# Performance work log

Hardware: AMD Instinct MI355X
Metric: run time of the kernel (lower is better)

Reference implementation:

```python
import jax, jax.numpy as jnp
import numpy as np

N_SAMPLES = 32768


def fft_shift(a, shift):
    n = a.shape[-1]
    shift_samples = shift * (n / 3.0)  # trailing dim of shift is 1 -> broadcasts over coeffs
    pad = [(0, 0)] * (a.ndim - 1) + [(0, 2 * n)]
    spec = jnp.fft.rfft(jnp.pad(a, pad), axis=-1, norm='ortho')
    n_coeffs = spec.shape[-1]
    phase = jnp.arange(n_coeffs) * (2j * jnp.pi / n_coeffs)
    spec = spec * jnp.exp(-phase * shift_samples)
    out = jnp.fft.irfft(spec, n=3 * n, axis=-1, norm='ortho')
    return out[..., :n]


def interp_linear(x, out_size):
    # matches torch F.interpolate(mode='linear', align_corners=False)
    in_size = x.shape[-1]
    scale = in_size / out_size
    coords = (jnp.arange(out_size, dtype=x.dtype) + 0.5) * scale - 0.5
    coords = jnp.clip(coords, 0.0, in_size - 1)
    i0 = jnp.floor(coords).astype(jnp.int32)
    i1 = jnp.minimum(i0 + 1, in_size - 1)
    w = coords - i0.astype(x.dtype)
    return x[..., i0] * (1.0 - w) + x[..., i1] * w


def instrument(t, shift, energy, properties):
    batch, n_events, time_len = t.shape
    t = fft_shift(t, shift)  # (b,e,T)
    _, _, cp, n_frames = energy.shape
    frame_shifts = jnp.linspace(0.0, 1.0, n_frames)
    # (b,e,1,T) shifted per-frame -> (b,e,F,T)
    exp_t = fft_shift(t[:, :, None, :], frame_shifts[None, None, :, None])
    exp_t = exp_t[:, :, None, :, :]  # (b,e,1,F,T)
    # triu mask with offset 2: mask[i,j]=1 iff j >= i+2
    mask = (jnp.arange(time_len)[None, :] >= (jnp.arange(n_frames)[:, None] + 2)).astype(t.dtype)
    mask = fft_shift(mask[None, None], shift[:, :, None, :])  # (b,e,F,T)
    mass = properties[..., :1, None]      # (b,e,cp,1,1)
    friction = properties[..., 1:, None]  # (b,e,cp,1,1)
    x = energy[..., None] * jnp.exp(-friction / (2.0 * mass) * exp_t)  # (b,e,cp,F,T)
    x = x * mask[:, :, None, :, :]
    return jnp.sum(x, axis=-2)  # (b,e,cp,T)


def reference(time, shifts, energy, shape, properties, w_pos, b_pos, w_layers, b_layers):
    batch, n_events, cp, n_frames = energy.shape
    channels, enc = w_pos.shape
    # positional filterbank -> embed -> (1,1,channels,N)
    freqs = jnp.linspace(1e-05, 0.5, enc)
    tt = jnp.linspace(0.0, float(N_SAMPLES), N_SAMPLES)
    p = jnp.sin(tt[:, None] * freqs[None, :] * jnp.pi)  # (N, enc)
    pos = (p @ w_pos.T + b_pos).T[None, None]  # (1,1,channels,N)
    # envelopes
    env = instrument(time, shifts, energy, properties)  # (b,e,cp,T)
    env = jax.nn.relu(interp_linear(env, N_SAMPLES))    # (b,e,cp,N)
    # shape network (residual layers use only l2: x + l2(relu(x)))
    s = jnp.swapaxes(shape, -1, -2)  # (b,e,F,channels)
    for i in range(w_layers.shape[0]):
        s = s + jax.nn.relu(s) @ w_layers[i].T + b_layers[i]
    s = jax.nn.relu(s)
    s = jnp.swapaxes(s, -1, -2)           # (b,e,channels,F)
    s = interp_linear(s, N_SAMPLES)       # (b,e,channels,N)
    x = pos * s * env                      # cp == channels
    return jnp.sum(x, axis=2)              # (b,e,N)


def setup_inputs():
    key = jax.random.key(0)
    ks = jax.random.split(key, 9)
    B, E, CP, F_, T, CH, ENC, L = 2, 8, 32, 64, 2048, 32, 256, 4
    return {
        'time': jax.random.uniform(ks[0], (B, E, T), dtype=jnp.float32),
        'shifts': jax.random.uniform(ks[1], (B, E, 1), dtype=jnp.float32),
        'energy': jax.random.uniform(ks[2], (B, E, CP, F_), dtype=jnp.float32),
        'shape': jax.random.normal(ks[3], (B, E, CH, F_), dtype=jnp.float32),
        'properties': jax.random.uniform(ks[4], (B, E, CP, 2), dtype=jnp.float32) + 0.5,
        'w_pos': jax.random.normal(ks[5], (CH, ENC), dtype=jnp.float32) * 0.06,
        'b_pos': jax.random.normal(ks[6], (CH,), dtype=jnp.float32) * 0.02,
        'w_layers': jax.random.normal(ks[7], (L, CH, CH), dtype=jnp.float32) * 0.15,
        'b_layers': jax.random.normal(ks[8], (L, CH), dtype=jnp.float32) * 0.02,
    }
```

## Files before the change

kernel.cpp:

```cpp
#include <hip/hip_runtime.h>
#include <math.h>

#define TL 2048
#define PI_D 3.14159265358979323846

typedef __attribute__((ext_vector_type(8))) short short8v;
typedef __attribute__((ext_vector_type(4))) float float4v;

#define REPLEN 392
#define REPB (REPLEN * 2)
#define OFF_B 8192

__device__ __forceinline__ unsigned short bf16_rne(float f) {
  unsigned u = __float_as_uint(f);
  return (unsigned short)((u + 0x7FFFu + ((u >> 16) & 1u)) >> 16);
}

__device__ __forceinline__ float tap_val(int idx, double beta, double wv) {
  int d = idx - 2047;
  double x = PI_D * (double)d / 6144.0 - beta;
  if (fabs(x) < 1e-9) return 1.0f;
  double c = wv * (cos(x) / sin(x));
  if (d & 1) c = -c;
  return (float)c;
}

__global__ __launch_bounds__(256) void build_shift_k(const float* __restrict__ shifts,
                                                     const float* __restrict__ time_in,
                                                     float* __restrict__ kerC,
                                                     unsigned short* __restrict__ BFrep,
                                                     unsigned short* __restrict__ tsh_b) {
  __shared__ __align__(16) unsigned char sm1[17408];
  __shared__ float wsum[4];
  int b = blockIdx.x;
  int tid = threadIdx.x;
  if (b < 80) {
    float* kf = (float*)sm1;
    double s;
    if (b < 64) s = (double)b * (1.0 / 63.0) * (2048.0 / 3.0);
    else        s = (double)shifts[b - 64] * (2048.0 / 3.0);
    double beta = PI_D * s / 3073.0;
    double y = 3072.0 * s / 3073.0;
    double r = y - rint(y);
    double wv = -sin(2.0 * PI_D * r) / 6144.0;
    for (int idx = tid; idx < 4104; idx += 256)
      kf[idx] = (idx < 4095) ? tap_val(idx, beta, wv) : 0.0f;
    __syncthreads();
    if (b < 64) {
      for (int c = tid; c < 4096; c += 256) {
        int sr = c >> 9;
        int m = c & 511;
        int A = 4095 - 8 * m + sr;
        unsigned short out[8];
#pragma unroll
        for (int rr = 0; rr < 8; ++rr) out[rr] = bf16_rne(kf[A - rr]);
        *(short8v*)(BFrep + ((size_t)(b * 8 + sr)) * 4104 + 8 * m) = *(short8v*)out;
      }
    } else {
      float s0 = 0.f;
      int base = tid * 16;
#pragma unroll
      for (int i = 0; i < 16; ++i) s0 += kf[base + i];
      int lane = tid & 63;
      float v = s0;
#pragma unroll
      for (int d = 1; d < 64; d <<= 1) {
        float o = __shfl_up(v, (unsigned)d, 64);
        if (lane >= d) v += o;
      }
      if (lane == 63) wsum[tid >> 6] = v;
      __syncthreads();
      float woff = 0.f;
      for (int k = 0; k < (tid >> 6); ++k) woff += wsum[k];
      float run = v + woff - s0;
      float* crow = kerC + (b - 64) * 4096;
#pragma unroll
      for (int i = 0; i < 16; ++i) {
        crow[base + i] = run;
        run += kf[base + i];
      }
    }
  } else {
    int pb = b - 80;
    int p = pb >> 3, tile = pb & 7;
    float* a = (float*)sm1;
    float* kw = (float*)(sm1 + 8192);
    int t0 = tile * 256;
    double s = (double)shifts[p] * (2048.0 / 3.0);
    double beta = PI_D * s / 3073.0;
    double y = 3072.0 * s / 3073.0;
    double r = y - rint(y);
    double wv = -sin(2.0 * PI_D * r) / 6144.0;
    for (int i = tid; i < 2048; i += 256) a[i] = time_in[p * 2048 + i];
    for (int i = tid; i < 2303; i += 256) kw[i] = tap_val(t0 + i, beta, wv);
    __syncthreads();
    float acc = 0.f;
    int base = tid + 2047;
#pragma unroll 8
    for (int u = 0; u < 2048; ++u) acc = fmaf(a[u], kw[base - u], acc);
    tsh_b[p * 2048 + t0 + tid] = bf16_rne(acc);
  }
}

__global__ __launch_bounds__(256, 4) void fused_k(const unsigned short* __restrict__ tsh_b,
                                                  const unsigned short* __restrict__ BFrep,
                                                  float* __restrict__ expT,
                                                  const float* __restrict__ w_pos,
                                                  const float* __restrict__ b_pos,
                                                  float* __restrict__ pos,
                                                  const float* __restrict__ shape,
                                                  const float* __restrict__ w_layers,
                                                  const float* __restrict__ b_layers,
                                                  float* __restrict__ s64) {
  __shared__ __align__(16) unsigned char smem[21248];
  int bx = blockIdx.x;
  int tid = threadIdx.x;
  if (bx < 1024) {
    int j = bx >> 4;
    int tB = (bx & 15) << 7;
    int l = tid & 63, w = tid >> 6;
    int p16 = l & 15, g = l >> 4;
    int srep = l & 7, hb = (l >> 3) & 1;
    int h = w >> 1, kp = w & 1;
    int kc0 = kp << 2;

    float4v acc[4];
#pragma unroll
    for (int i = 0; i < 4; ++i) acc[i] = (float4v){0.f, 0.f, 0.f, 0.f};
    int bB2 = OFF_B + srep * REPB + 256 - (hb << 4) + (g << 4) - (h << 7);
    const unsigned short* grow = BFrep + (size_t)j * 8 * 4104;

    for (int ph = 0; ph < 8; ++ph) {
      int ub = ph << 8;
      int Q8 = 1912 - tB + ub;
      __syncthreads();
#pragma unroll
      for (int it = 0; it < 2; ++it) {
        int c = tid + (it << 8);
        int pp = c >> 5, m = c & 31;
        short8v v = *(const short8v*)(tsh_b + pp * 2048 + ub + (m << 3));
        int dst = ((pp << 9) + (m << 4)) ^ ((pp & 7) << 4);
        *(short8v*)(smem + dst) = v;
      }
      for (int c = tid; c < 384; c += 256) {
        int sr = c / 48;
        int m = c - sr * 48;
        short8v v = *(const short8v*)(grow + sr * 4104 + 8 + Q8 + (m << 3));
        *(short8v*)(smem + OFF_B + sr * REPB + (m << 4)) = v;
      }
      __syncthreads();
      int fb = bB2 + (kc0 << 6);
      short8v W0 = *(const short8v*)(smem + fb);
      short8v W1 = *(const short8v*)(smem + fb - 32);
      short8v W2 = *(const short8v*)(smem + fb - 64);
      short8v W3 = *(const short8v*)(smem + fb - 96);
#pragma unroll
      for (int qq = 0; qq < 4; ++qq) {
        int kc = kc0 + qq;
        if (qq > 0) {
          short8v t2 = W0, t3 = W1;
          W0 = *(const short8v*)(smem + fb + (qq << 6));
          W1 = *(const short8v*)(smem + fb + (qq << 6) - 32);
          W2 = t2;
          W3 = t3;
        }
        int ao = ((p16 << 9) + (kc << 6) + (g << 4)) ^ ((p16 & 7) << 4);
        short8v a = *(const short8v*)(smem + ao);
        acc[0] = __builtin_amdgcn_mfma_f32_16x16x32_bf16(a, W0, acc[0], 0, 0, 0);
        acc[1] = __builtin_amdgcn_mfma_f32_16x16x32_bf16(a, W1, acc[1], 0, 0, 0);
        acc[2] = __builtin_amdgcn_mfma_f32_16x16x32_bf16(a, W2, acc[2], 0, 0, 0);
        acc[3] = __builtin_amdgcn_mfma_f32_16x16x32_bf16(a, W3, acc[3], 0, 0, 0);
      }
    }
    __syncthreads();
    if (kp == 1) {
#pragma unroll
      for (int ct = 0; ct < 4; ++ct)
        *(float4v*)(smem + ((((h << 2) + ct) << 6) + l) * 16) = acc[ct];
    }
    __syncthreads();
    if (kp == 0) {
#pragma unroll
      for (int ct = 0; ct < 4; ++ct) {
        float4v o = *(const float4v*)(smem + ((((h << 2) + ct) << 6) + l) * 16);
#pragma unroll
        for (int rr = 0; rr < 4; ++rr) acc[ct][rr] += o[rr];
      }
      int tbase = tB + (h << 6) + p16;
#pragma unroll
      for (int ct = 0; ct < 4; ++ct) {
#pragma unroll
        for (int rr = 0; rr < 4; ++rr) {
          int prow = (g << 2) + rr;
          expT[(size_t)(prow * 64 + j) * TL + tbase + (ct << 4)] = acc[ct][rr];
        }
      }
    }
  } else if (bx < 1536) {
    int l = tid & 63, w = tid >> 6;
    int p16 = l & 15, g = l >> 4;
    int T0 = (bx - 1024) * 64 + w * 16;

    float ttv = (float)(T0 + p16) * (32768.0f / 32767.0f);
    float4v acc0 = {0.f, 0.f, 0.f, 0.f};
    float4v acc1 = {0.f, 0.f, 0.f, 0.f};
#pragma unroll
    for (int kc = 0; kc < 8; ++kc) {
      short8v bh0, bl0, bh1, bl1;
#pragma unroll
      for (int ct = 0; ct < 2; ++ct) {
        const float* wrow = w_pos + (ct * 16 + p16) * 256 + kc * 32 + g * 8;
        float4v w0 = *(const float4v*)(wrow);
        float4v w1 = *(const float4v*)(wrow + 4);
        short8v hv, lv;
#pragma unroll
        for (int i = 0; i < 8; ++i) {
          float vv = (i < 4) ? w0[i] : w1[i - 4];
          unsigned short hbit = bf16_rne(vv);
          float hf = __uint_as_float(((unsigned)hbit) << 16);
          hv[i] = (short)hbit;
          lv[i] = (short)bf16_rne(vv - hf);
        }
        if (ct == 0) { bh0 = hv; bl0 = lv; }
        else         { bh1 = hv; bl1 = lv; }
      }
      short8v ahi, alo;
#pragma unroll
      for (int i = 0; i < 8; ++i) {
        int f = kc * 32 + g * 8 + i;
        float fr = 1e-5f + (float)f * ((0.5f - 1e-5f) / 255.0f);
        float rev = ttv * (0.5f * fr);
        float sv = __builtin_amdgcn_sinf(__builtin_amdgcn_fractf(rev));
        unsigned short hbit = bf16_rne(sv);
        float hf = __uint_as_float(((unsigned)hbit) << 16);
        ahi[i] = (short)hbit;
        alo[i] = (short)bf16_rne(sv - hf);
      }
      acc0 = __builtin_amdgcn_mfma_f32_16x16x32_bf16(ahi, bh0, acc0, 0, 0, 0);
      acc1 = __builtin_amdgcn_mfma_f32_16x16x32_bf16(ahi, bh1, acc1, 0, 0, 0);
      acc0 = __builtin_amdgcn_mfma_f32_16x16x32_bf16(ahi, bl0, acc0, 0, 0, 0);
      acc1 = __builtin_amdgcn_mfma_f32_16x16x32_bf16(ahi, bl1, acc1, 0, 0, 0);
      acc0 = __builtin_amdgcn_mfma_f32_16x16x32_bf16(alo, bh0, acc0, 0, 0, 0);
      acc1 = __builtin_amdgcn_mfma_f32_16x16x32_bf16(alo, bh1, acc1, 0, 0, 0);
    }
    float bp0 = b_pos[p16], bp1 = b_pos[16 + p16];
    float4v o0, o1;
#pragma unroll
    for (int rr = 0; rr < 4; ++rr) {
      o0[rr] = acc0[rr] + bp0;
      o1[rr] = acc1[rr] + bp1;
    }
    int Tr = T0 + g * 4;
    *(float4v*)(pos + (size_t)p16 * 32768 + Tr) = o0;
    *(float4v*)(pos + (size_t)(16 + p16) * 32768 + Tr) = o1;
  } else {
    float(*sA)[33] = (float(*)[33])(smem);
    float(*sB)[33] = (float(*)[33])(smem + 8448);
    float(*W)[33] = (float(*)[33])(smem + 16896);
    float* bb = (float*)(smem + 21120);
    int p = bx - 1536;
    for (int idx = tid; idx < 2048; idx += 256) {
      int c = idx >> 6, f = idx & 63;
      sA[f][c] = shape[p * 2048 + idx];
    }
    int c = tid & 31, fg = tid >> 5;
    for (int ll = 0; ll < 4; ++ll) {
      for (int idx = tid; idx < 1024; idx += 256) W[idx >> 5][idx & 31] = w_layers[ll * 1024 + idx];
      if (tid < 32) bb[tid] = b_layers[ll * 32 + tid];
      __syncthreads();
      float(*cur)[33] = (ll & 1) ? sB : sA;
      float(*nxt)[33] = (ll & 1) ? sA : sB;
#pragma unroll
      for (int i = 0; i < 8; ++i) {
        int f = fg * 8 + i;
        float acc = cur[f][c] + bb[c];
#pragma unroll
        for (int k = 0; k < 32; ++k) acc = fmaf(fmaxf(cur[f][k], 0.f), W[c][k], acc);
        nxt[f][c] = acc;
      }
      __syncthreads();
    }
    for (int idx = tid; idx < 2048; idx += 256) {
      int cc = idx >> 6, f = idx & 63;
      s64[p * 2048 + idx] = fmaxf(sA[f][cc], 0.f);
    }
  }
}

__global__ __launch_bounds__(256) void env2_k(const float* __restrict__ energy,
                                              const float* __restrict__ props,
                                              const float* __restrict__ expT,
                                              const float* __restrict__ kerC,
                                              float* __restrict__ env) {
  int p = blockIdx.x >> 5, tile = blockIdx.x & 31;
  int tl = threadIdx.x & 63;
  int cg = threadIdx.x >> 6;
  int tC = tile * 64;
  int t = tC + tl;
  __shared__ float E[32][64];
  __shared__ float K[32];
  __shared__ float kcl[2112];
  for (int i = threadIdx.x; i < 2048; i += 256) E[i >> 6][i & 63] = energy[p * 2048 + i];
  const float* crow = kerC + p * 4096;
  for (int i = threadIdx.x; i < 2110; i += 256) kcl[i] = crow[tC + i];
  if (threadIdx.x < 32) {
    float mass = props[(p * 32 + threadIdx.x) * 2];
    float fric = props[(p * 32 + threadIdx.x) * 2 + 1];
    K[threadIdx.x] = fric / (2.0f * mass);
  }
  __syncthreads();
  float acc[8];
  float kk[8];
#pragma unroll
  for (int i = 0; i < 8; ++i) acc[i] = 0.f;
#pragma unroll
  for (int i = 0; i < 8; ++i) kk[i] = K[cg * 8 + i];
  float Ct = kcl[tl];
  const float* xrow = expT + (size_t)p * 64 * TL + t;
  for (int jj = 0; jj < 64; ++jj) {
    float x = xrow[jj * TL];
    float mv = kcl[tl + 2046 - jj] - Ct;
#pragma unroll
    for (int cc = 0; cc < 8; ++cc)
      acc[cc] = fmaf(E[cg * 8 + cc][jj] * mv, __expf(-kk[cc] * x), acc[cc]);
  }
#pragma unroll
  for (int cc = 0; cc < 8; ++cc)
    env[(size_t)(p * 32 + cg * 8 + cc) * TL + t] = acc[cc];
}

__global__ __launch_bounds__(256) void final_k(const float* __restrict__ pos,
                                               const float* __restrict__ s64,
                                               const float* __restrict__ env,
                                               float* __restrict__ out) {
  int gid = blockIdx.x * 256 + threadIdx.x;
  int p = gid >> 15, T = gid & 32767;
  float ft = (float)T + 0.5f;
  float ce = fminf(fmaxf(ft * 0.0625f - 0.5f, 0.f), 2047.f);
  int ie = (int)ce;
  int ie1 = min(ie + 1, 2047);
  float we = ce - (float)ie;
  float cs = fminf(fmaxf(ft * (1.0f / 512.0f) - 0.5f, 0.f), 63.f);
  int is0 = (int)cs;
  int is1 = min(is0 + 1, 63);
  float ws = cs - (float)is0;
  const float* erow = env + (size_t)p * 32 * TL;
  const float* srow = s64 + p * 32 * 64;
  float acc = 0.f;
  for (int c = 0; c < 32; ++c) {
    float pv = pos[(size_t)c * 32768 + T];
    float ev = fmaxf(erow[c * TL + ie] * (1.f - we) + erow[c * TL + ie1] * we, 0.f);
    float sv = srow[c * 64 + is0] * (1.f - ws) + srow[c * 64 + is1] * ws;
    acc += pv * sv * ev;
  }
  out[gid] = acc;
}

extern "C" void kernel_launch(void* const* d_in, const int* in_sizes, int n_in,
                              void* d_out, int out_size, void* d_ws, size_t ws_size,
                              hipStream_t stream) {
  const float* time_in  = (const float*)d_in[0];
  const float* shifts   = (const float*)d_in[1];
  const float* energy   = (const float*)d_in[2];
  const float* shape    = (const float*)d_in[3];
  const float* props    = (const float*)d_in[4];
  const float* w_pos    = (const float*)d_in[5];
  const float* b_pos    = (const float*)d_in[6];
  const float* w_layers = (const float*)d_in[7];
  const float* b_layers = (const float*)d_in[8];

  float* ws = (float*)d_ws;
  float* kerC = ws;
  unsigned short* BFrep = (unsigned short*)(ws + 65536);
  unsigned short* tsh_b = (unsigned short*)(ws + 1116160);
  float* expT = ws + 1132544;
  float* env  = ws + 3229696;
  float* pos  = ws + 4278272;
  float* s64  = ws + 5326848;
  float* out  = (float*)d_out;

  hipLaunchKernelGGL(build_shift_k, dim3(208), dim3(256), 0, stream,
                     shifts, time_in, kerC, BFrep, tsh_b);
  hipLaunchKernelGGL(fused_k, dim3(1552), dim3(256), 0, stream, tsh_b, BFrep, expT,
                     w_pos, b_pos, pos, shape, w_layers, b_layers, s64);
  hipLaunchKernelGGL(env2_k, dim3(512), dim3(256), 0, stream, energy, props, expT, kerC, env);
  hipLaunchKernelGGL(final_k, dim3(2048), dim3(256), 0, stream, pos, s64, env, out);
}
```

Before: 102.9 us.

## Double-buffer A tiles via direct global-to-LDS loads and preload full B window

The shift convolution in build_shift_k is split across two half-warpsets with a shared-memory reduction, doubling its block count, and it now writes the bf16 result in a pre-swizzled layout. In fused2_k, each block loads its whole B Toeplitz window once up front. The A tiles are double-buffered with global_load_lds so the next phase's load overlaps the current MFMA work and one barrier per phase is dropped. The small MLP blocks are moved ahead of the positional blocks so they start early. The trade is larger LDS use per block, the occupancy hint is removed, and the new path relies on the swizzle layout being right.

```diff
diff --git a/kernel.cpp b/kernel.cpp
--- a/kernel.cpp
+++ b/kernel.cpp
@@ -7,9 +7,8 @@
 typedef __attribute__((ext_vector_type(8))) short short8v;
 typedef __attribute__((ext_vector_type(4))) float float4v;
 
-#define REPLEN 392
-#define REPB (REPLEN * 2)
-#define OFF_B 8192
+#define B_OFF 16384
+#define BRS 4368
 
 __device__ __forceinline__ unsigned short bf16_rne(float f) {
   unsigned u = __float_as_uint(f);
@@ -29,7 +28,7 @@
                                                      const float* __restrict__ time_in,
                                                      float* __restrict__ kerC,
                                                      unsigned short* __restrict__ BFrep,
-                                                     unsigned short* __restrict__ tsh_b) {
+                                                     unsigned short* __restrict__ tsh_swz) {
   __shared__ __align__(16) unsigned char sm1[17408];
   __shared__ float wsum[4];
   int b = blockIdx.x;
@@ -81,38 +80,51 @@
       }
     }
   } else {
-    int pb = b - 80;
-    int p = pb >> 3, tile = pb & 7;
+    int idx = b - 80;
+    int p = idx >> 4, tile = idx & 15;
+    int t0 = tile * 128;
     float* a = (float*)sm1;
     float* kw = (float*)(sm1 + 8192);
-    int t0 = tile * 256;
+    float* partial = (float*)(sm1 + 16896);
     double s = (double)shifts[p] * (2048.0 / 3.0);
     double beta = PI_D * s / 3073.0;
     double y = 3072.0 * s / 3073.0;
     double r = y - rint(y);
     double wv = -sin(2.0 * PI_D * r) / 6144.0;
     for (int i = tid; i < 2048; i += 256) a[i] = time_in[p * 2048 + i];
-    for (int i = tid; i < 2303; i += 256) kw[i] = tap_val(t0 + i, beta, wv);
-    __syncthreads();
+    for (int i = tid; i < 2175; i += 256) kw[i] = tap_val(t0 + i, beta, wv);
+    __syncthreads();
+    int tl = tid & 127, uh = tid >> 7;
+    int base = tl + 2047 - (uh << 10);
+    int u0 = uh << 10;
     float acc = 0.f;
-    int base = tid + 2047;
 #pragma unroll 8
-    for (int u = 0; u < 2048; ++u) acc = fmaf(a[u], kw[base - u], acc);
-    tsh_b[p * 2048 + t0 + tid] = bf16_rne(acc);
+    for (int u2 = 0; u2 < 1024; ++u2) acc = fmaf(a[u0 + u2], kw[base - u2], acc);
+    __syncthreads();
+    if (uh == 1) partial[tl] = acc;
+    __syncthreads();
+    if (uh == 0) {
+      acc += partial[tl];
+      int t = t0 + tl;
+      int phh = t >> 8, up = t & 255;
+      int m = up >> 3, i2 = up & 7;
+      int D = (p << 5) | (m ^ (p & 7));
+      tsh_swz[phh * 4096 + D * 8 + i2] = bf16_rne(acc);
+    }
   }
 }
 
-__global__ __launch_bounds__(256, 4) void fused_k(const unsigned short* __restrict__ tsh_b,
-                                                  const unsigned short* __restrict__ BFrep,
-                                                  float* __restrict__ expT,
-                                                  const float* __restrict__ w_pos,
-                                                  const float* __restrict__ b_pos,
-                                                  float* __restrict__ pos,
-                                                  const float* __restrict__ shape,
-                                                  const float* __restrict__ w_layers,
-                                                  const float* __restrict__ b_layers,
-                                                  float* __restrict__ s64) {
-  __shared__ __align__(16) unsigned char smem[21248];
+__global__ __launch_bounds__(256) void fused2_k(const unsigned short* __restrict__ tsh_swz,
+                                                const unsigned short* __restrict__ BFrep,
+                                                float* __restrict__ expT,
+                                                const float* __restrict__ w_pos,
+                                                const float* __restrict__ b_pos,
+                                                float* __restrict__ pos,
+                                                const float* __restrict__ shape,
+                                                const float* __restrict__ w_layers,
+                                                const float* __restrict__ b_layers,
+                                                float* __restrict__ s64) {
+  __shared__ __align__(16) unsigned char smem[16384 + 8 * BRS];
   int bx = blockIdx.x;
   int tid = threadIdx.x;
   if (bx < 1024) {
@@ -123,33 +135,39 @@
     int srep = l & 7, hb = (l >> 3) & 1;
     int h = w >> 1, kp = w & 1;
     int kc0 = kp << 2;
+    int z_lo = 1920 - tB;
+    const unsigned short* grow = BFrep + (size_t)j * 8 * 4104;
+
+#pragma unroll
+    for (int sr = 0; sr < 8; ++sr) {
+      for (int m = tid; m < 272; m += 256) {
+        short8v v = *(const short8v*)(grow + sr * 4104 + z_lo + (m << 3));
+        *(short8v*)(smem + B_OFF + sr * BRS + (m << 4)) = v;
+      }
+    }
+    auto stage_a = [&](int buf, int ph2) {
+#pragma unroll
+      for (int it = 0; it < 2; ++it) {
+        const unsigned int* src =
+            (const unsigned int*)tsh_swz + ((ph2 << 11) + (((it << 8) + tid) << 2));
+        unsigned char* dstp = smem + buf * 8192 + (it << 12) + ((tid >> 6) << 10);
+        __builtin_amdgcn_global_load_lds(
+            (const __attribute__((address_space(1))) unsigned int*)src,
+            (__attribute__((address_space(3))) unsigned int*)dstp, 16, 0, 0);
+      }
+    };
+    stage_a(0, 0);
+    __syncthreads();
 
     float4v acc[4];
 #pragma unroll
     for (int i = 0; i < 4; ++i) acc[i] = (float4v){0.f, 0.f, 0.f, 0.f};
-    int bB2 = OFF_B + srep * REPB + 256 - (hb << 4) + (g << 4) - (h << 7);
-    const unsigned short* grow = BFrep + (size_t)j * 8 * 4104;
+    int bB2 = B_OFF + srep * BRS + 256 - (hb << 4) + (g << 4) - (h << 7);
+    int cur = 0;
 
     for (int ph = 0; ph < 8; ++ph) {
-      int ub = ph << 8;
-      int Q8 = 1912 - tB + ub;
-      __syncthreads();
-#pragma unroll
-      for (int it = 0; it < 2; ++it) {
-        int c = tid + (it << 8);
-        int pp = c >> 5, m = c & 31;
-        short8v v = *(const short8v*)(tsh_b + pp * 2048 + ub + (m << 3));
-        int dst = ((pp << 9) + (m << 4)) ^ ((pp & 7) << 4);
-        *(short8v*)(smem + dst) = v;
-      }
-      for (int c = tid; c < 384; c += 256) {
-        int sr = c / 48;
-        int m = c - sr * 48;
-        short8v v = *(const short8v*)(grow + sr * 4104 + 8 + Q8 + (m << 3));
-        *(short8v*)(smem + OFF_B + sr * REPB + (m << 4)) = v;
-      }
-      __syncthreads();
-      int fb = bB2 + (kc0 << 6);
+      if (ph < 7) stage_a(cur ^ 1, ph + 1);
+      int fb = bB2 + (ph << 9) + (kc0 << 6);
       short8v W0 = *(const short8v*)(smem + fb);
       short8v W1 = *(const short8v*)(smem + fb - 32);
       short8v W2 = *(const short8v*)(smem + fb - 64);
@@ -164,15 +182,16 @@
           W2 = t2;
           W3 = t3;
         }
-        int ao = ((p16 << 9) + (kc << 6) + (g << 4)) ^ ((p16 & 7) << 4);
+        int ao = cur * 8192 + (((p16 << 9) + (kc << 6) + (g << 4)) ^ ((p16 & 7) << 4));
         short8v a = *(const short8v*)(smem + ao);
         acc[0] = __builtin_amdgcn_mfma_f32_16x16x32_bf16(a, W0, acc[0], 0, 0, 0);
         acc[1] = __builtin_amdgcn_mfma_f32_16x16x32_bf16(a, W1, acc[1], 0, 0, 0);
         acc[2] = __builtin_amdgcn_mfma_f32_16x16x32_bf16(a, W2, acc[2], 0, 0, 0);
         acc[3] = __builtin_amdgcn_mfma_f32_16x16x32_bf16(a, W3, acc[3], 0, 0, 0);
       }
-    }
-    __syncthreads();
+      __syncthreads();
+      cur ^= 1;
+    }
     if (kp == 1) {
 #pragma unroll
       for (int ct = 0; ct < 4; ++ct)
@@ -196,10 +215,41 @@
         }
       }
     }
-  } else if (bx < 1536) {
+  } else if (bx < 1040) {
+    float(*sA)[33] = (float(*)[33])(smem);
+    float(*sB)[33] = (float(*)[33])(smem + 8448);
+    float(*W)[33] = (float(*)[33])(smem + 16896);
+    float* bb = (float*)(smem + 21120);
+    int p = bx - 1024;
+    for (int idx = tid; idx < 2048; idx += 256) {
+      int c = idx >> 6, f = idx & 63;
+      sA[f][c] = shape[p * 2048 + idx];
+    }
+    int c = tid & 31, fg = tid >> 5;
+    for (int ll = 0; ll < 4; ++ll) {
+      for (int idx = tid; idx < 1024; idx += 256) W[idx >> 5][idx & 31] = w_layers[ll * 1024 + idx];
+      if (tid < 32) bb[tid] = b_layers[ll * 32 + tid];
+      __syncthreads();
+      float(*cur)[33] = (ll & 1) ? sB : sA;
+      float(*nxt)[33] = (ll & 1) ? sA : sB;
+#pragma unroll
+      for (int i = 0; i < 8; ++i) {
+        int f = fg * 8 + i;
+        float acc = cur[f][c] + bb[c];
+#pragma unroll
+        for (int k = 0; k < 32; ++k) acc = fmaf(fmaxf(cur[f][k], 0.f), W[c][k], acc);
+        nxt[f][c] = acc;
+      }
+      __syncthreads();
+    }
+    for (int idx = tid; idx < 2048; idx += 256) {
+      int cc = idx >> 6, f = idx & 63;
+      s64[p * 2048 + idx] = fmaxf(sA[f][cc], 0.f);
+    }
+  } else {
     int l = tid & 63, w = tid >> 6;
     int p16 = l & 15, g = l >> 4;
-    int T0 = (bx - 1024) * 64 + w * 16;
+    int T0 = (bx - 1040) * 64 + w * 16;
 
     float ttv = (float)(T0 + p16) * (32768.0f / 32767.0f);
     float4v acc0 = {0.f, 0.f, 0.f, 0.f};
@@ -253,37 +303,6 @@
     int Tr = T0 + g * 4;
     *(float4v*)(pos + (size_t)p16 * 32768 + Tr) = o0;
     *(float4v*)(pos + (size_t)(16 + p16) * 32768 + Tr) = o1;
-  } else {
-    float(*sA)[33] = (float(*)[33])(smem);
-    float(*sB)[33] = (float(*)[33])(smem + 8448);
-    float(*W)[33] = (float(*)[33])(smem + 16896);
-    float* bb = (float*)(smem + 21120);
-    int p = bx - 1536;
-    for (int idx = tid; idx < 2048; idx += 256) {
-      int c = idx >> 6, f = idx & 63;
-      sA[f][c] = shape[p * 2048 + idx];
-    }
-    int c = tid & 31, fg = tid >> 5;
-    for (int ll = 0; ll < 4; ++ll) {
-      for (int idx = tid; idx < 1024; idx += 256) W[idx >> 5][idx & 31] = w_layers[ll * 1024 + idx];
-      if (tid < 32) bb[tid] = b_layers[ll * 32 + tid];
-      __syncthreads();
-      float(*cur)[33] = (ll & 1) ? sB : sA;
-      float(*nxt)[33] = (ll & 1) ? sA : sB;
-#pragma unroll
-      for (int i = 0; i < 8; ++i) {
-        int f = fg * 8 + i;
-        float acc = cur[f][c] + bb[c];
-#pragma unroll
-        for (int k = 0; k < 32; ++k) acc = fmaf(fmaxf(cur[f][k], 0.f), W[c][k], acc);
-        nxt[f][c] = acc;
-      }
-      __syncthreads();
-    }
-    for (int idx = tid; idx < 2048; idx += 256) {
-      int cc = idx >> 6, f = idx & 63;
-      s64[p * 2048 + idx] = fmaxf(sA[f][cc], 0.f);
-    }
   }
 }
 
@@ -372,16 +391,16 @@
   float* ws = (float*)d_ws;
   float* kerC = ws;
   unsigned short* BFrep = (unsigned short*)(ws + 65536);
-  unsigned short* tsh_b = (unsigned short*)(ws + 1116160);
+  unsigned short* tsh_swz = (unsigned short*)(ws + 1116160);
   float* expT = ws + 1132544;
   float* env  = ws + 3229696;
   float* pos  = ws + 4278272;
   float* s64  = ws + 5326848;
   float* out  = (float*)d_out;
 
-  hipLaunchKernelGGL(build_shift_k, dim3(208), dim3(256), 0, stream,
-                     shifts, time_in, kerC, BFrep, tsh_b);
-  hipLaunchKernelGGL(fused_k, dim3(1552), dim3(256), 0, stream, tsh_b, BFrep, expT,
+  hipLaunchKernelGGL(build_shift_k, dim3(336), dim3(256), 0, stream,
+                     shifts, time_in, kerC, BFrep, tsh_swz);
+  hipLaunchKernelGGL(fused2_k, dim3(1552), dim3(256), 0, stream, tsh_swz, BFrep, expT,
                      w_pos, b_pos, pos, shape, w_layers, b_layers, s64);
   hipLaunchKernelGGL(env2_k, dim3(512), dim3(256), 0, stream, energy, props, expT, kerC, env);
   hipLaunchKernelGGL(final_k, dim3(2048), dim3(256), 0, stream, pos, s64, env, out);
```

Measured after the change: 108.8 us. 5.8% more time.
